# Kernel optimization log

Hardware: AMD Instinct MI355X
Metric: run time of the kernel (lower is better)

Reference implementation:

```python
import jax, jax.numpy as jnp
import numpy as np

B, S, D, H, DH = 2, 2048, 1024, 16, 64
SCALE = float(np.sqrt(DH))
IGNORE = -100000.0


def setup_inputs() -> dict:
    key = jax.random.key(0)
    ks = jax.random.split(key, 9)
    s = 0.02
    return {
        "x": jax.random.normal(ks[0], (B, S, D), dtype=jnp.float32),
        "W_Q": jax.random.normal(ks[1], (H, DH, D), dtype=jnp.float32) * s,
        "W_K": jax.random.normal(ks[2], (H, DH, D), dtype=jnp.float32) * s,
        "W_V": jax.random.normal(ks[3], (H, DH, D), dtype=jnp.float32) * s,
        "W_O": jax.random.normal(ks[4], (H, D, DH), dtype=jnp.float32) * s,
        "b_Q": jax.random.normal(ks[5], (H, DH), dtype=jnp.float32) * s,
        "b_K": jax.random.normal(ks[6], (H, DH), dtype=jnp.float32) * s,
        "b_V": jax.random.normal(ks[7], (H, DH), dtype=jnp.float32) * s,
        "b_O": jax.random.normal(ks[8], (D,), dtype=jnp.float32) * s,
        "mask": jnp.tril(jnp.ones((S, S), dtype=bool)),  # causal, global attn_type
    }


def reference(x, W_Q, W_K, W_V, W_O, b_Q, b_K, b_V, b_O, mask):
    # q,k,v: [batch, pos, head, d_head]
    q = jnp.einsum('ihm,bpm->bpih', W_Q, x) + b_Q
    k = jnp.einsum('ihm,bpm->bpih', W_K, x) + b_K
    v = jnp.einsum('ihm,bpm->bpih', W_V, x) + b_V
    # scores: [batch, head, q_pos, k_pos]
    attn_scores = jnp.einsum('bpih,bqih->bipq', q, k) / SCALE
    attn_scores = jnp.where(mask, attn_scores, IGNORE)
    attn = jax.nn.softmax(attn_scores, axis=-1)
    # z: [batch, q_pos, head, d_head]
    z = jnp.einsum('bpih,biqp->bqih', v, attn)
    out = jnp.einsum('idh,bqih->bqd', W_O, z) + b_O
    return out
```

## Files before the change

kernel.cpp:

```cpp
#include <hip/hip_runtime.h>
#include <stdint.h>

typedef __attribute__((ext_vector_type(8))) short bf16x8;
typedef __attribute__((ext_vector_type(4))) float f32x4;
typedef __attribute__((ext_vector_type(16))) float f32x16;
typedef __attribute__((ext_vector_type(4))) unsigned short us4;

#define LOG2E 1.44269504088896340736f

__device__ __forceinline__ unsigned short f2bf(float f) {
    union { float f; unsigned u; } v; v.f = f;
    unsigned r = v.u + 0x7FFFu + ((v.u >> 16) & 1u);
    return (unsigned short)(r >> 16);
}
__device__ __forceinline__ float bf2f(unsigned short u) {
    return __uint_as_float(((unsigned)u) << 16);
}

__device__ __forceinline__ unsigned cvtpk(float lo, float hi) {
    unsigned r;
    asm("v_cvt_pk_bf16_f32 %0, %1, %2" : "=v"(r) : "v"(lo), "v"(hi));
    return r;
}
__device__ __forceinline__ void plswap(unsigned &a, unsigned &b) {
    asm volatile("v_permlane32_swap_b32 %0, %1" : "+v"(a), "+v"(b));
}

__device__ __forceinline__ void gld16(const void* g, void* l) {
    __builtin_amdgcn_global_load_lds((const __attribute__((address_space(1))) void*)g,
                                     (__attribute__((address_space(3))) void*)l, 16, 0, 0);
}

__global__ void k_cvt_all(
    const float* __restrict__ x,  const float* __restrict__ WQ,
    const float* __restrict__ WK, const float* __restrict__ WV,
    const float* __restrict__ WO,
    unsigned short* __restrict__ xb,  unsigned short* __restrict__ wqb,
    unsigned short* __restrict__ wkb, unsigned short* __restrict__ wvb,
    unsigned short* __restrict__ wob)
{
    const int blk = blockIdx.x;
    if (blk < 7168) {
        const float* in; unsigned short* out; int base;
        if (blk < 4096)      { in = x;  out = xb;  base = blk; }
        else if (blk < 5120) { in = WQ; out = wqb; base = blk - 4096; }
        else if (blk < 6144) { in = WK; out = wkb; base = blk - 5120; }
        else                 { in = WV; out = wvb; base = blk - 6144; }
        int i = base * 256 + threadIdx.x;
        float4 v = ((const float4*)in)[i];
        us4 o; o.x = f2bf(v.x); o.y = f2bf(v.y); o.z = f2bf(v.z); o.w = f2bf(v.w);
        *(us4*)(out + (size_t)i * 4) = o;
    } else {
        int t = (blk - 7168) * 256 + threadIdx.x;
        int d = t >> 10, nn = t & 1023, i = nn >> 6, h = nn & 63;
        wob[t] = f2bf(WO[(((size_t)i << 10) + d) * 64 + h]);
    }
}

__global__ __launch_bounds__(256) void k_gemm_qkv(
    const unsigned short* __restrict__ Xb,
    const unsigned short* __restrict__ Wq, const unsigned short* __restrict__ Wk,
    const unsigned short* __restrict__ Wv,
    const float* __restrict__ bQ, const float* __restrict__ bK, const float* __restrict__ bV,
    unsigned short* __restrict__ Qb, unsigned short* __restrict__ Kb, unsigned short* __restrict__ VTb)
{
    __shared__ unsigned short As[128][128];
    __shared__ unsigned short Bs[128][128];
    const int which = blockIdx.z;
    const unsigned short* Wp = which == 0 ? Wq : (which == 1 ? Wk : Wv);
    const int bm = blockIdx.x, bn = blockIdx.y;
    const int t = threadIdx.x, lane = t & 63, wave = t >> 6;
    const int wm = wave >> 1, wn = wave & 1;
    const int l15 = lane & 15, l4 = lane >> 4;
    const int rsw = l15 & 7;
    const int c0 = wave * 64 + lane;
    const int arow = bm << 7, brow = bn << 7;
    f32x4 acc[4][4] = {};

    for (int k0 = 0; k0 < 1024; k0 += 128) {
        #pragma unroll
        for (int it = 0; it < 8; ++it) {
            int c = it * 256 + c0;
            int row = c >> 4, sl = (c & 15) ^ (row & 7);
            gld16(Xb + ((size_t)(arow + row)) * 1024 + k0 + sl * 8, (char*)As + (c << 4));
            gld16(Wp + ((size_t)(brow + row)) * 1024 + k0 + sl * 8, (char*)Bs + (c << 4));
        }
        __syncthreads();
        const char* Ab = (const char*)As;
        const char* Bb = (const char*)Bs;
        #pragma unroll
        for (int kk = 0; kk < 4; ++kk) {
            bf16x8 af[4], bfg[4];
            #pragma unroll
            for (int m = 0; m < 4; ++m)
                af[m] = *(const bf16x8*)(Ab + (wm * 64 + m * 16 + l15) * 256 + (((kk * 4 + l4) ^ rsw) << 4));
            #pragma unroll
            for (int n = 0; n < 4; ++n)
                bfg[n] = *(const bf16x8*)(Bb + (wn * 64 + n * 16 + l15) * 256 + (((kk * 4 + l4) ^ rsw) << 4));
            __builtin_amdgcn_s_setprio(1);
            #pragma unroll
            for (int m = 0; m < 4; ++m)
                #pragma unroll
                for (int n = 0; n < 4; ++n)
                    acc[m][n] = __builtin_amdgcn_mfma_f32_16x16x32_bf16(af[m], bfg[n], acc[m][n], 0, 0, 0);
            __builtin_amdgcn_s_setprio(0);
        }
        __syncthreads();
    }
    #pragma unroll
    for (int m = 0; m < 4; ++m) {
        #pragma unroll
        for (int n = 0; n < 4; ++n) {
            int col = (bn << 7) + wn * 64 + n * 16 + l15;
            int i = col >> 6, h = col & 63;
            float bias = which == 0 ? bQ[col] : (which == 1 ? bK[col] : bV[col]);
            #pragma unroll
            for (int r = 0; r < 4; ++r) {
                int p = (bm << 7) + wm * 64 + m * 16 + (l4 << 2) + r;
                int b = p >> 11, s = p & 2047;
                float v = acc[m][n][r] + bias;
                if (which == 0)
                    Qb[(((((size_t)b << 4) + i) << 11) + s) * 64 + h] = f2bf(v * (0.125f * LOG2E));
                else if (which == 1)
                    Kb[(((((size_t)b << 4) + i) << 11) + s) * 64 + h] = f2bf(v);
                else
                    VTb[(((((size_t)b << 4) + i) << 6) + h) * 2048 + s] = f2bf(v);
            }
        }
    }
}

__global__ __launch_bounds__(128) void k_attn(
    const unsigned short* __restrict__ Qb, const unsigned short* __restrict__ Kb,
    const unsigned short* __restrict__ VTb,
    unsigned short* __restrict__ Zp, float* __restrict__ Lse)
{
    __shared__ __align__(16) char Lbuf[16384];
    const int id = (int)blockIdx.x;
    const int bi = id & 31;
    const int r = id >> 5;
    const int c = 31 - (r >> 1);
    const int part = r & 1;
    const int n = c + 1, n0 = (n + 1) >> 1;
    const int t0 = part ? n0 : 0, t1 = part ? n : n0;
    const int lane = threadIdx.x & 63, w = threadIdx.x >> 6;
    const int l31 = lane & 31, hi = lane >> 5;
    const unsigned short* Qh = Qb + (size_t)bi * 2048 * 64;
    const char* Khb = (const char*)(Kb + (size_t)bi * 2048 * 64);
    const char* Vhb = (const char*)(VTb + (size_t)bi * 64 * 2048);
    const int q0 = c * 64 + w * 32;
    const int q = q0 + l31;

    bf16x8 qf[4];
    #pragma unroll
    for (int kk = 0; kk < 4; ++kk)
        qf[kk] = *(const bf16x8*)&Qh[(size_t)q * 64 + kk * 16 + hi * 8];

    const int r8 = lane >> 3;
    const int swz = ((lane & 7) * 16) ^ (r8 << 4);
    const int koff = r8 * 128 + swz;
    const int voff = r8 * 4096 + swz;

    const int rsw = (l31 & 7) << 4;
    int kaddr[8];
    #pragma unroll
    for (int i = 0; i < 8; ++i)
        kaddr[i] = (l31 + 32 * (i >> 2)) * 128 + ((32 * (i & 3) + 16 * hi) ^ rsw);
    int vcol[4];
    #pragma unroll
    for (int f = 0; f < 4; ++f)
        vcol[f] = ((f * 32 + 16 * hi) ^ rsw);

    f32x16 za0 = {}, za1 = {};
    float m_run = -1e30f, l_run = 0.f;

    if (t0 < t1) {
        if (w == 0) {
            const char* src = Khb + (size_t)t0 * 8192 + koff;
            #pragma unroll
            for (int it = 0; it < 8; ++it) gld16(src + it * 1024, &Lbuf[0] + it * 1024);
        } else {
            const char* src = Vhb + (size_t)t0 * 128 + voff;
            #pragma unroll
            for (int it = 0; it < 8; ++it) gld16(src + it * 32768, &Lbuf[8192] + it * 1024);
        }
    }

    for (int t = t0; t < t1; ++t) {
        __syncthreads();
        const char* KL = &Lbuf[0];
        const char* VL = &Lbuf[8192];
        bf16x8 ka[8];
        #pragma unroll
        for (int i = 0; i < 8; ++i) ka[i] = *(const bf16x8*)(KL + kaddr[i]);
        bf16x8 vf0[4], vf1[4];
        #pragma unroll
        for (int f = 0; f < 4; ++f) {
            vf0[f] = *(const bf16x8*)(VL + l31 * 128 + vcol[f]);
            vf1[f] = *(const bf16x8*)(VL + (l31 + 32) * 128 + vcol[f]);
        }
        __syncthreads();
        if (t + 1 < t1) {
            if (w == 0) {
                const char* src = Khb + (size_t)(t + 1) * 8192 + koff;
                #pragma unroll
                for (int it = 0; it < 8; ++it) gld16(src + it * 1024, &Lbuf[0] + it * 1024);
            } else {
                const char* src = Vhb + (size_t)(t + 1) * 128 + voff;
                #pragma unroll
                for (int it = 0; it < 8; ++it) gld16(src + it * 32768, &Lbuf[8192] + it * 1024);
            }
        }

        const bool full = !(t == c && w == 0);
        f32x16 s0 = {}, s1;
        __builtin_amdgcn_s_setprio(1);
        #pragma unroll
        for (int kk = 0; kk < 4; ++kk)
            s0 = __builtin_amdgcn_mfma_f32_32x32x16_bf16(ka[kk], qf[kk], s0, 0, 0, 0);
        if (full) {
            f32x16 z = {};
            #pragma unroll
            for (int kk = 0; kk < 4; ++kk)
                z = __builtin_amdgcn_mfma_f32_32x32x16_bf16(ka[4 + kk], qf[kk], z, 0, 0, 0);
            s1 = z;
        }
        __builtin_amdgcn_s_setprio(0);

        if (!full) {
            #pragma unroll
            for (int j = 0; j < 16; ++j) s1[j] = -100000.0f;
        }
        if (t == c) {
            #pragma unroll
            for (int j = 0; j < 16; ++j) {
                int kv0 = (j & 3) + 8 * (j >> 2) + 4 * hi;
                if (c * 64 + kv0 > q) s0[j] = -100000.0f;
                if (c * 64 + kv0 + 32 > q) s1[j] = -100000.0f;
            }
        }
        float tmax = -1e30f;
        #pragma unroll
        for (int j = 0; j < 16; ++j) tmax = fmaxf(tmax, fmaxf(s0[j], s1[j]));
        tmax = fmaxf(tmax, __shfl_xor(tmax, 32, 64));
        if (!__all(tmax <= m_run + 8.0f)) {
            float newm = fmaxf(m_run, tmax);
            float alpha = exp2f(m_run - newm);
            m_run = newm;
            l_run *= alpha;
            za0 *= alpha; za1 *= alpha;
        }
        float rsum = 0.f;
        #pragma unroll
        for (int j = 0; j < 16; ++j) { s0[j] = exp2f(s0[j] - m_run); rsum += s0[j]; }
        if (full) {
            #pragma unroll
            for (int j = 0; j < 16; ++j) { s1[j] = exp2f(s1[j] - m_run); rsum += s1[j]; }
        }
        rsum += __shfl_xor(rsum, 32, 64);
        l_run += rsum;

        union { unsigned u[4]; bf16x8 v; } pk0, pk1, pk2, pk3;
        {
            unsigned a0 = cvtpk(s0[0], s0[1]),  a1 = cvtpk(s0[2], s0[3]);
            unsigned a2 = cvtpk(s0[4], s0[5]),  a3 = cvtpk(s0[6], s0[7]);
            plswap(a0, a2); plswap(a1, a3);
            pk0.u[0] = a0; pk0.u[1] = a1; pk0.u[2] = a2; pk0.u[3] = a3;
            unsigned b0 = cvtpk(s0[8], s0[9]),  b1 = cvtpk(s0[10], s0[11]);
            unsigned b2 = cvtpk(s0[12], s0[13]), b3 = cvtpk(s0[14], s0[15]);
            plswap(b0, b2); plswap(b1, b3);
            pk1.u[0] = b0; pk1.u[1] = b1; pk1.u[2] = b2; pk1.u[3] = b3;
        }
        if (full) {
            unsigned a0 = cvtpk(s1[0], s1[1]),  a1 = cvtpk(s1[2], s1[3]);
            unsigned a2 = cvtpk(s1[4], s1[5]),  a3 = cvtpk(s1[6], s1[7]);
            plswap(a0, a2); plswap(a1, a3);
            pk2.u[0] = a0; pk2.u[1] = a1; pk2.u[2] = a2; pk2.u[3] = a3;
            unsigned b0 = cvtpk(s1[8], s1[9]),  b1 = cvtpk(s1[10], s1[11]);
            unsigned b2 = cvtpk(s1[12], s1[13]), b3 = cvtpk(s1[14], s1[15]);
            plswap(b0, b2); plswap(b1, b3);
            pk3.u[0] = b0; pk3.u[1] = b1; pk3.u[2] = b2; pk3.u[3] = b3;
        }
        __builtin_amdgcn_s_setprio(1);
        za0 = __builtin_amdgcn_mfma_f32_32x32x16_bf16(vf0[0], pk0.v, za0, 0, 0, 0);
        za1 = __builtin_amdgcn_mfma_f32_32x32x16_bf16(vf1[0], pk0.v, za1, 0, 0, 0);
        za0 = __builtin_amdgcn_mfma_f32_32x32x16_bf16(vf0[1], pk1.v, za0, 0, 0, 0);
        za1 = __builtin_amdgcn_mfma_f32_32x32x16_bf16(vf1[1], pk1.v, za1, 0, 0, 0);
        if (full) {
            za0 = __builtin_amdgcn_mfma_f32_32x32x16_bf16(vf0[2], pk2.v, za0, 0, 0, 0);
            za1 = __builtin_amdgcn_mfma_f32_32x32x16_bf16(vf1[2], pk2.v, za1, 0, 0, 0);
            za0 = __builtin_amdgcn_mfma_f32_32x32x16_bf16(vf0[3], pk3.v, za0, 0, 0, 0);
            za1 = __builtin_amdgcn_mfma_f32_32x32x16_bf16(vf1[3], pk3.v, za1, 0, 0, 0);
        }
        __builtin_amdgcn_s_setprio(0);
    }

    const float rl = (l_run > 0.f) ? 1.0f / l_run : 0.f;
    const float lse = (l_run > 0.f) ? m_run + log2f(l_run) : -1e30f;
    const int pb = (part << 5) + bi;
    unsigned short* zp = Zp + ((size_t)pb * 2048 + q) * 64;
    #pragma unroll
    for (int nn = 0; nn < 2; ++nn) {
        #pragma unroll
        for (int gg = 0; gg < 4; ++gg) {
            int dh0 = nn * 32 + 8 * gg + 4 * hi;
            us4 o;
            float v0 = (nn ? za1[4 * gg + 0] : za0[4 * gg + 0]) * rl;
            float v1 = (nn ? za1[4 * gg + 1] : za0[4 * gg + 1]) * rl;
            float v2 = (nn ? za1[4 * gg + 2] : za0[4 * gg + 2]) * rl;
            float v3 = (nn ? za1[4 * gg + 3] : za0[4 * gg + 3]) * rl;
            o.x = f2bf(v0); o.y = f2bf(v1); o.z = f2bf(v2); o.w = f2bf(v3);
            *(us4*)(zp + dh0) = o;
        }
    }
    if (hi == 0) Lse[(size_t)pb * 2048 + q] = lse;
}

__global__ __launch_bounds__(256) void k_combine(
    const unsigned short* __restrict__ Zp, const float* __restrict__ Lse,
    unsigned short* __restrict__ Zb)
{
    const int tid = blockIdx.x * 256 + threadIdx.x;
    const int dc = tid & 7, q = (tid >> 3) & 2047, bi = tid >> 14;
    const float l0 = Lse[(size_t)bi * 2048 + q];
    const float l1 = Lse[(size_t)(32 + bi) * 2048 + q];
    const float M = fmaxf(l0, l1);
    float e0 = exp2f(l0 - M), e1 = exp2f(l1 - M);
    const float rs = 1.0f / (e0 + e1);
    e0 *= rs; e1 *= rs;
    const size_t base = ((size_t)bi * 2048 + q) * 64 + dc * 8;
    bf16x8 z0 = *(const bf16x8*)(Zp + base);
    bf16x8 z1 = *(const bf16x8*)(Zp + (size_t)32 * 2048 * 64 + base);
    const int b = bi >> 4, ih = bi & 15;
    unsigned short* op = Zb + (((size_t)b * 2048 + q) << 10) + ih * 64 + dc * 8;
    bf16x8 o;
    #pragma unroll
    for (int j = 0; j < 8; ++j) {
        float v = e0 * bf2f((unsigned short)z0[j]) + e1 * bf2f((unsigned short)z1[j]);
        o[j] = (short)f2bf(v);
    }
    *(bf16x8*)op = o;
}

__global__ __launch_bounds__(256) void k_gemm_out(
    const unsigned short* __restrict__ Zb, const unsigned short* __restrict__ Wo,
    const float* __restrict__ bO, float* __restrict__ out)
{
    __shared__ unsigned short As[128][128];
    __shared__ unsigned short Bs[128][128];
    const int bm = blockIdx.x, bn = blockIdx.y;
    const int t = threadIdx.x, lane = t & 63, wave = t >> 6;
    const int wm = wave >> 1, wn = wave & 1;
    const int l15 = lane & 15, l4 = lane >> 4;
    const int rsw = l15 & 7;
    const int c0 = wave * 64 + lane;
    const int arow = bm << 7, brow = bn << 7;
    f32x4 acc[4][4] = {};

    for (int k0 = 0; k0 < 1024; k0 += 128) {
        #pragma unroll
        for (int it = 0; it < 8; ++it) {
            int c = it * 256 + c0;
            int row = c >> 4, sl = (c & 15) ^ (row & 7);
            gld16(Zb + ((size_t)(arow + row)) * 1024 + k0 + sl * 8, (char*)As + (c << 4));
            gld16(Wo + ((size_t)(brow + row)) * 1024 + k0 + sl * 8, (char*)Bs + (c << 4));
        }
        __syncthreads();
        const char* Ab = (const char*)As;
        const char* Bb = (const char*)Bs;
        #pragma unroll
        for (int kk = 0; kk < 4; ++kk) {
            bf16x8 af[4], bfg[4];
            #pragma unroll
            for (int m = 0; m < 4; ++m)
                af[m] = *(const bf16x8*)(Ab + (wm * 64 + m * 16 + l15) * 256 + (((kk * 4 + l4) ^ rsw) << 4));
            #pragma unroll
            for (int n = 0; n < 4; ++n)
                bfg[n] = *(const bf16x8*)(Bb + (wn * 64 + n * 16 + l15) * 256 + (((kk * 4 + l4) ^ rsw) << 4));
            __builtin_amdgcn_s_setprio(1);
            #pragma unroll
            for (int m = 0; m < 4; ++m)
                #pragma unroll
                for (int n = 0; n < 4; ++n)
                    acc[m][n] = __builtin_amdgcn_mfma_f32_16x16x32_bf16(af[m], bfg[n], acc[m][n], 0, 0, 0);
            __builtin_amdgcn_s_setprio(0);
        }
        __syncthreads();
    }
    #pragma unroll
    for (int m = 0; m < 4; ++m) {
        #pragma unroll
        for (int n = 0; n < 4; ++n) {
            int col = (bn << 7) + wn * 64 + n * 16 + l15;
            float bias = bO[col];
            #pragma unroll
            for (int r = 0; r < 4; ++r) {
                int p = (bm << 7) + wm * 64 + m * 16 + (l4 << 2) + r;
                out[(size_t)p * 1024 + col] = acc[m][n][r] + bias;
            }
        }
    }
}

extern "C" void kernel_launch(void* const* d_in, const int* in_sizes, int n_in,
                              void* d_out, int out_size, void* d_ws, size_t ws_size,
                              hipStream_t stream)
{
    const float* x  = (const float*)d_in[0];
    const float* WQ = (const float*)d_in[1];
    const float* WK = (const float*)d_in[2];
    const float* WV = (const float*)d_in[3];
    const float* WO = (const float*)d_in[4];
    const float* bQ = (const float*)d_in[5];
    const float* bK = (const float*)d_in[6];
    const float* bV = (const float*)d_in[7];
    const float* bO = (const float*)d_in[8];
    float* out = (float*)d_out;

    char* w = (char*)d_ws;
    unsigned short* xb  = (unsigned short*)w; w += (size_t)4096 * 1024 * 2;
    unsigned short* wqb = (unsigned short*)w; w += (size_t)1024 * 1024 * 2;
    unsigned short* wkb = (unsigned short*)w; w += (size_t)1024 * 1024 * 2;
    unsigned short* wvb = (unsigned short*)w; w += (size_t)1024 * 1024 * 2;
    unsigned short* wob = (unsigned short*)w; w += (size_t)1024 * 1024 * 2;
    unsigned short* Qb  = (unsigned short*)w; w += (size_t)4096 * 1024 * 2;
    unsigned short* Kb  = (unsigned short*)w; w += (size_t)4096 * 1024 * 2;
    unsigned short* VTb = (unsigned short*)w; w += (size_t)4096 * 1024 * 2;
    unsigned short* Zb  = (unsigned short*)w; w += (size_t)4096 * 1024 * 2;
    unsigned short* Zp  = (unsigned short*)w; w += (size_t)2 * 32 * 2048 * 64 * 2;
    float*          Lse = (float*)w;          w += (size_t)2 * 32 * 2048 * 4;

    k_cvt_all<<<11264, 256, 0, stream>>>(x, WQ, WK, WV, WO, xb, wqb, wkb, wvb, wob);

    k_gemm_qkv<<<dim3(32, 8, 3), 256, 0, stream>>>(xb, wqb, wkb, wvb, bQ, bK, bV, Qb, Kb, VTb);
    k_attn<<<2048, 128, 0, stream>>>(Qb, Kb, VTb, Zp, Lse);
    k_combine<<<2048, 256, 0, stream>>>(Zp, Lse, Zb);
    k_gemm_out<<<dim3(32, 8), 256, 0, stream>>>(Zb, wob, bO, out);
}
```

Measured before the change: 127.0 us.

## Widen attention blocks to 128 queries sharing each K/V tile

The attention kernel now runs four waves per block, covering 128 query rows instead of 64, with half as many blocks. Every wave reads the same staged K/V tile, so global and LDS-fill traffic per query roughly halves, and the cooperative load is spread across all 256 threads. Along the causal diagonal, waves whose queries sit before the current KV tile skip compute but still take part in the barriers. That leaves some idle waves and reduces the number of blocks available to balance work across CUs.

```diff
diff --git a/kernel.cpp b/kernel.cpp
--- a/kernel.cpp
+++ b/kernel.cpp
@@ -130,7 +130,7 @@
     }
 }
 
-__global__ __launch_bounds__(128) void k_attn(
+__global__ __launch_bounds__(256) void k_attn(
     const unsigned short* __restrict__ Qb, const unsigned short* __restrict__ Kb,
     const unsigned short* __restrict__ VTb,
     unsigned short* __restrict__ Zp, float* __restrict__ Lse)
@@ -139,27 +139,23 @@
     const int id = (int)blockIdx.x;
     const int bi = id & 31;
     const int r = id >> 5;
-    const int c = 31 - (r >> 1);
+    const int g = 15 - (r >> 1);
     const int part = r & 1;
-    const int n = c + 1, n0 = (n + 1) >> 1;
-    const int t0 = part ? n0 : 0, t1 = part ? n : n0;
-    const int lane = threadIdx.x & 63, w = threadIdx.x >> 6;
+    const int t0 = part * (g + 1), t1 = t0 + g + 1;
+    const int tid = threadIdx.x;
+    const int lane = tid & 63, w = tid >> 6;
     const int l31 = lane & 31, hi = lane >> 5;
+    const int sgrp = tid & 127;
     const unsigned short* Qh = Qb + (size_t)bi * 2048 * 64;
     const char* Khb = (const char*)(Kb + (size_t)bi * 2048 * 64);
     const char* Vhb = (const char*)(VTb + (size_t)bi * 64 * 2048);
-    const int q0 = c * 64 + w * 32;
-    const int q = q0 + l31;
+    const int q = g * 128 + w * 32 + l31;
+    const int dq = q >> 6;
 
     bf16x8 qf[4];
     #pragma unroll
     for (int kk = 0; kk < 4; ++kk)
         qf[kk] = *(const bf16x8*)&Qh[(size_t)q * 64 + kk * 16 + hi * 8];
-
-    const int r8 = lane >> 3;
-    const int swz = ((lane & 7) * 16) ^ (r8 << 4);
-    const int koff = r8 * 128 + swz;
-    const int voff = r8 * 4096 + swz;
 
     const int rsw = (l31 & 7) << 4;
     int kaddr[8];
@@ -174,45 +170,64 @@
     f32x16 za0 = {}, za1 = {};
     float m_run = -1e30f, l_run = 0.f;
 
-    if (t0 < t1) {
-        if (w == 0) {
-            const char* src = Khb + (size_t)t0 * 8192 + koff;
-            #pragma unroll
-            for (int it = 0; it < 8; ++it) gld16(src + it * 1024, &Lbuf[0] + it * 1024);
+    {
+        if (w < 2) {
+            const char* src = Khb + (size_t)t0 * 8192;
+            #pragma unroll
+            for (int it = 0; it < 4; ++it) {
+                int cc = it * 128 + sgrp;
+                int row = cc >> 3, j = cc & 7;
+                gld16(src + row * 128 + ((j * 16) ^ ((row & 7) << 4)), &Lbuf[0] + cc * 16);
+            }
         } else {
-            const char* src = Vhb + (size_t)t0 * 128 + voff;
-            #pragma unroll
-            for (int it = 0; it < 8; ++it) gld16(src + it * 32768, &Lbuf[8192] + it * 1024);
+            const char* src = Vhb + (size_t)t0 * 128;
+            #pragma unroll
+            for (int it = 0; it < 4; ++it) {
+                int cc = it * 128 + sgrp;
+                int row = cc >> 3, j = cc & 7;
+                gld16(src + (size_t)row * 4096 + ((j * 16) ^ ((row & 7) << 4)), &Lbuf[8192] + cc * 16);
+            }
         }
     }
 
     for (int t = t0; t < t1; ++t) {
-        __syncthreads();
-        const char* KL = &Lbuf[0];
-        const char* VL = &Lbuf[8192];
-        bf16x8 ka[8];
-        #pragma unroll
-        for (int i = 0; i < 8; ++i) ka[i] = *(const bf16x8*)(KL + kaddr[i]);
-        bf16x8 vf0[4], vf1[4];
-        #pragma unroll
-        for (int f = 0; f < 4; ++f) {
-            vf0[f] = *(const bf16x8*)(VL + l31 * 128 + vcol[f]);
-            vf1[f] = *(const bf16x8*)(VL + (l31 + 32) * 128 + vcol[f]);
+        const bool active = (t <= dq);
+        __syncthreads();
+        bf16x8 ka[8], vf0[4], vf1[4];
+        if (active) {
+            const char* KL = &Lbuf[0];
+            const char* VL = &Lbuf[8192];
+            #pragma unroll
+            for (int i = 0; i < 8; ++i) ka[i] = *(const bf16x8*)(KL + kaddr[i]);
+            #pragma unroll
+            for (int f = 0; f < 4; ++f) {
+                vf0[f] = *(const bf16x8*)(VL + l31 * 128 + vcol[f]);
+                vf1[f] = *(const bf16x8*)(VL + (l31 + 32) * 128 + vcol[f]);
+            }
         }
         __syncthreads();
         if (t + 1 < t1) {
-            if (w == 0) {
-                const char* src = Khb + (size_t)(t + 1) * 8192 + koff;
+            if (w < 2) {
+                const char* src = Khb + (size_t)(t + 1) * 8192;
                 #pragma unroll
-                for (int it = 0; it < 8; ++it) gld16(src + it * 1024, &Lbuf[0] + it * 1024);
+                for (int it = 0; it < 4; ++it) {
+                    int cc = it * 128 + sgrp;
+                    int row = cc >> 3, j = cc & 7;
+                    gld16(src + row * 128 + ((j * 16) ^ ((row & 7) << 4)), &Lbuf[0] + cc * 16);
+                }
             } else {
-                const char* src = Vhb + (size_t)(t + 1) * 128 + voff;
+                const char* src = Vhb + (size_t)(t + 1) * 128;
                 #pragma unroll
-                for (int it = 0; it < 8; ++it) gld16(src + it * 32768, &Lbuf[8192] + it * 1024);
-            }
-        }
-
-        const bool full = !(t == c && w == 0);
+                for (int it = 0; it < 4; ++it) {
+                    int cc = it * 128 + sgrp;
+                    int row = cc >> 3, j = cc & 7;
+                    gld16(src + (size_t)row * 4096 + ((j * 16) ^ ((row & 7) << 4)), &Lbuf[8192] + cc * 16);
+                }
+            }
+        }
+        if (!active) continue;
+
+        const bool full = !(t == dq && ((w & 1) == 0));
         f32x16 s0 = {}, s1;
         __builtin_amdgcn_s_setprio(1);
         #pragma unroll
@@ -231,12 +246,12 @@
             #pragma unroll
             for (int j = 0; j < 16; ++j) s1[j] = -100000.0f;
         }
-        if (t == c) {
+        if (t == dq) {
             #pragma unroll
             for (int j = 0; j < 16; ++j) {
                 int kv0 = (j & 3) + 8 * (j >> 2) + 4 * hi;
-                if (c * 64 + kv0 > q) s0[j] = -100000.0f;
-                if (c * 64 + kv0 + 32 > q) s1[j] = -100000.0f;
+                if (t * 64 + kv0 > q) s0[j] = -100000.0f;
+                if (t * 64 + kv0 + 32 > q) s1[j] = -100000.0f;
             }
         }
         float tmax = -1e30f;
@@ -433,7 +448,7 @@
     k_cvt_all<<<11264, 256, 0, stream>>>(x, WQ, WK, WV, WO, xb, wqb, wkb, wvb, wob);
 
     k_gemm_qkv<<<dim3(32, 8, 3), 256, 0, stream>>>(xb, wqb, wkb, wvb, bQ, bK, bV, Qb, Kb, VTb);
-    k_attn<<<2048, 128, 0, stream>>>(Qb, Kb, VTb, Zp, Lse);
+    k_attn<<<1024, 256, 0, stream>>>(Qb, Kb, VTb, Zp, Lse);
     k_combine<<<2048, 256, 0, stream>>>(Zp, Lse, Zb);
     k_gemm_out<<<dim3(32, 8), 256, 0, stream>>>(Zb, wob, bO, out);
 }
```

Result: slower. 149.0 us (+17.3%).
